# Kernel optimization log

Measured on AMD Instinct MI355X. Metric: run time of the kernel, lower is better.

The kernel has to match this reference:

```python
import jax, jax.numpy as jnp
import numpy as np

# hyperparameters (from init_kwargs)
DIM = 192; NH = 6; WS = 16; SHIFT = 8; M = 64; RC = 10; CS = 256; KS = 5
HID = DIM * 2  # mlp_ratio = 2


def _layernorm(x, g, b, eps=1e-5):
    mu = jnp.mean(x, axis=-1, keepdims=True)
    var = jnp.var(x, axis=-1, keepdims=True)
    return (x - mu) * jax.lax.rsqrt(var + eps) * g + b


def _window_partition(x, ws):
    b, h, w, c = x.shape
    x = x.reshape(b, h // ws, ws, w // ws, ws, c)
    return x.transpose(0, 1, 3, 2, 4, 5).reshape(-1, ws, ws, c)


def _window_reverse(win, ws, h, w):
    b = win.shape[0] // ((h // ws) * (w // ws))
    x = win.reshape(b, h // ws, w // ws, ws, ws, -1)
    return x.transpose(0, 1, 3, 2, 4, 5).reshape(b, h, w, -1)


def setup_inputs() -> dict:
    key = jax.random.key(0)
    ks = jax.random.split(key, 24)
    b, h, w = 2, 192, 192
    n = h * w
    f32 = jnp.float32
    rn = lambda k, shape, s=0.02: (jax.random.normal(k, shape) * s).astype(f32)
    inp = {}
    inp['x'] = jax.random.normal(ks[0], (b, n, DIM), f32)
    inp['td'] = jax.random.normal(ks[1], (b, M, DIM), f32)
    # relative position index (standard Swin construction)
    coords = np.stack(np.meshgrid(np.arange(WS), np.arange(WS), indexing='ij')).reshape(2, -1)
    rel = (coords[:, :, None] - coords[:, None, :]).transpose(1, 2, 0).astype(np.int64)
    rel[:, :, 0] += WS - 1; rel[:, :, 1] += WS - 1
    rel[:, :, 0] *= 2 * WS - 1
    inp['rpi_sa'] = jnp.asarray(rel.sum(-1), jnp.int32)  # (ws^2, ws^2)
    # shifted-window attention mask (0 / -100)
    img_mask = np.zeros((1, h, w, 1), np.float32)
    cnt = 0
    for hs in (slice(0, -WS), slice(-WS, -SHIFT), slice(-SHIFT, None)):
        for wsl in (slice(0, -WS), slice(-WS, -SHIFT), slice(-SHIFT, None)):
            img_mask[:, hs, wsl, :] = cnt; cnt += 1
    mw = np.asarray(_window_partition(jnp.asarray(img_mask), WS)).reshape(-1, WS * WS)
    am = mw[:, None, :] - mw[:, :, None]
    inp['attn_mask'] = jnp.asarray(np.where(am != 0, -100.0, 0.0).astype(np.float32))  # (nw, ws^2, ws^2)
    inp['h'] = h; inp['w'] = w
    # parameters
    inp['norm1_g'] = jnp.ones((DIM,), f32); inp['norm1_b'] = jnp.zeros((DIM,), f32)
    inp['norm2_g'] = jnp.ones((DIM,), f32); inp['norm2_b'] = jnp.zeros((DIM,), f32)
    inp['norm3_g'] = jnp.ones((DIM,), f32); inp['norm3_b'] = jnp.zeros((DIM,), f32)
    inp['wqkv_w'] = rn(ks[2], (DIM, 3 * DIM)); inp['wqkv_b'] = jnp.zeros((3 * DIM,), f32)
    inp['wq_w'] = rn(ks[3], (DIM, RC)); inp['wq_b'] = jnp.zeros((RC,), f32)
    inp['wk_w'] = rn(ks[4], (DIM, RC)); inp['wk_b'] = jnp.zeros((RC,), f32)
    inp['wv_w'] = rn(ks[5], (DIM, DIM)); inp['wv_b'] = jnp.zeros((DIM,), f32)
    inp['atd_scale'] = 0.5 * jnp.ones((M,), f32)
    inp['proj_aca_w'] = rn(ks[6], (DIM, DIM)); inp['proj_aca_b'] = jnp.zeros((DIM,), f32)
    inp['logit_scale'] = jnp.full((1, 1), np.log(10.0), f32)
    inp['rpb_table'] = rn(ks[7], ((2 * WS - 1) ** 2, NH))
    inp['proj_win_w'] = rn(ks[8], (DIM, DIM)); inp['proj_win_b'] = jnp.zeros((DIM,), f32)
    inp['fc1_w'] = rn(ks[9], (DIM, HID)); inp['fc1_b'] = jnp.zeros((HID,), f32)
    inp['dw_w'] = rn(ks[10], (HID, 1, KS, KS)); inp['dw_b'] = jnp.zeros((HID,), f32)
    inp['fc2_w'] = rn(ks[11], (HID, DIM)); inp['fc2_b'] = jnp.zeros((DIM,), f32)
    inp['sigma'] = jnp.zeros((M, 1), f32)
    return inp


def reference(x, td, rpi_sa, attn_mask, h, w,
              norm1_g, norm1_b, norm2_g, norm2_b, norm3_g, norm3_b,
              wqkv_w, wqkv_b, wq_w, wq_b, wk_w, wk_b, wv_w, wv_b, atd_scale,
              proj_aca_w, proj_aca_b, logit_scale, rpb_table, proj_win_w, proj_win_b,
              fc1_w, fc1_b, dw_w, dw_b, fc2_w, fc2_b, sigma):
    b, n, c = x.shape
    hd = c // NH
    shortcut = x
    xn = _layernorm(x, norm1_g, norm1_b)
    qkv = xn @ wqkv_w + wqkv_b  # (b, n, 3c)

    # ----- ATD_CA: token-dictionary cross attention -----
    q = xn @ wq_w + wq_b                              # (b, n, rc)
    k = td @ wk_w + wk_b                              # (b, m, rc)
    v = td @ wv_w + wv_b                              # (b, m, c)
    qn = q / jnp.maximum(jnp.linalg.norm(q, axis=-1, keepdims=True), 1e-12)
    kn = k / jnp.maximum(jnp.linalg.norm(k, axis=-1, keepdims=True), 1e-12)
    attn = jnp.einsum('bnr,bmr->bnm', qn, kn)
    attn = attn * (1.0 + jnp.clip(atd_scale, 0.0, 1.0) * np.float32(np.log(M)))
    sim_atd = jax.nn.softmax(attn, axis=-1)           # (b, n, m)
    x_atd = jnp.einsum('bnm,bmc->bnc', sim_atd, v)

    # ----- AC_MSA: category sort + grouped attention -----
    gs = min(n, CS); ng = (n + gs - 1) // gs; pad_n = ng * gs - n
    tk_id = jnp.argmax(sim_atd, axis=-1)              # (b, n)
    sort_idx = jnp.argsort(tk_id, axis=-1)
    inv_idx = jnp.argsort(sort_idx, axis=-1)
    shuf = jnp.take_along_axis(qkv, sort_idx[:, :, None], axis=1)
    padded = jnp.concatenate([shuf, shuf[:, n - pad_n:n, :][:, ::-1, :]], axis=1)
    y = padded.reshape(b, ng, gs, 3, NH, hd).transpose(3, 0, 1, 4, 2, 5)  # (3,b,ng,nh,gs,hd)
    qg, kg, vg = y[0], y[1], y[2]
    ls = jnp.exp(jnp.minimum(logit_scale, np.float32(np.log(100.0))))
    ag = jax.nn.softmax(jnp.einsum('bgnqd,bgnkd->bgnqk', qg, kg) * ls, axis=-1)
    x_aca = jnp.einsum('bgnqk,bgnkd->bgnqd', ag, vg).transpose(0, 1, 3, 2, 4).reshape(b, ng * gs, c)[:, :n]
    x_aca = jnp.take_along_axis(x_aca, inv_idx[:, :, None], axis=1)
    x_aca = x_aca @ proj_aca_w + proj_aca_b

    # ----- shifted-window MSA -----
    qkv_img = qkv.reshape(b, h, w, 3 * c)
    shifted = jnp.roll(qkv_img, (-SHIFT, -SHIFT), axis=(1, 2))
    wins = _window_partition(shifted, WS).reshape(-1, WS * WS, 3 * c)
    b_, nt = wins.shape[0], WS * WS
    qkvw = wins.reshape(b_, nt, 3, NH, hd).transpose(2, 0, 3, 1, 4)
    qw = qkvw[0] * (hd ** -0.5); kw = qkvw[1]; vw = qkvw[2]
    aw = jnp.einsum('bhqd,bhkd->bhqk', qw, kw)
    rpb = rpb_table[rpi_sa.reshape(-1)].reshape(nt, nt, NH).transpose(2, 0, 1)
    aw = aw + rpb[None]
    nw = attn_mask.shape[0]
    aw = (aw.reshape(b_ // nw, nw, NH, nt, nt) + attn_mask[None, :, None]).reshape(b_, NH, nt, nt)
    aw = jax.nn.softmax(aw, axis=-1)
    ow = jnp.einsum('bhqk,bhkd->bhqd', aw, vw).transpose(0, 2, 1, 3).reshape(b_, nt, c)
    ow = ow @ proj_win_w + proj_win_b
    shifted_x = _window_reverse(ow.reshape(-1, WS, WS, c), WS, h, w)
    x_win = jnp.roll(shifted_x, (SHIFT, SHIFT), axis=(1, 2)).reshape(b, n, c)

    x = shortcut + x_win + x_atd + x_aca

    # ----- ConvFFN -----
    y2 = _layernorm(x, norm2_g, norm2_b)
    y2 = jax.nn.gelu(y2 @ fc1_w + fc1_b, approximate=False)
    img = y2.transpose(0, 2, 1).reshape(b, HID, h, w)
    cv = jax.lax.conv_general_dilated(img, dw_w, (1, 1), [(KS // 2, KS // 2)] * 2,
                                      feature_group_count=HID)
    cv = jax.nn.gelu(cv + dw_b[None, :, None, None], approximate=False)
    y2 = y2 + cv.reshape(b, HID, n).transpose(0, 2, 1)
    x = x + (y2 @ fc2_w + fc2_b)

    # ----- adaptive token dictionary refinement -----
    mask_soft = jax.nn.softmax(sim_atd.transpose(0, 2, 1), axis=-1)  # (b, m, n)
    s = jax.nn.sigmoid(sigma)  # (m, 1)
    td_new = s * td + (1.0 - s) * jnp.einsum('bmn,bnc->bmc', mask_soft,
                                             _layernorm(x, norm3_g, norm3_b))
    return x, td_new
```

## Files before the change

### kernel.cpp

```cpp
#include <hip/hip_runtime.h>
#include <math.h>

#define BB 2
#define HH 192
#define WW 192
#define NN 36864
#define CC 192
#define NHEAD 6
#define HD 32
#define MM 64
#define RC 10
#define GS 256
#define NG 144
#define HID 384
#define BN 73728

typedef unsigned short u16;
typedef __attribute__((ext_vector_type(8))) short short8;
typedef __attribute__((ext_vector_type(4))) float f32x4;

__device__ __forceinline__ float b2f(u16 u) { return __uint_as_float(((unsigned)u) << 16); }
__device__ __forceinline__ u16 f2b(float f) {
  unsigned v = __float_as_uint(f);
  return (u16)((v + 0x7fffu + ((v >> 16) & 1u)) >> 16);
}
__device__ __forceinline__ void up8(uint4 u, float* f) {
  f[0] = __uint_as_float(u.x << 16); f[1] = __uint_as_float(u.x & 0xffff0000u);
  f[2] = __uint_as_float(u.y << 16); f[3] = __uint_as_float(u.y & 0xffff0000u);
  f[4] = __uint_as_float(u.z << 16); f[5] = __uint_as_float(u.z & 0xffff0000u);
  f[6] = __uint_as_float(u.w << 16); f[7] = __uint_as_float(u.w & 0xffff0000u);
}
__device__ __forceinline__ float gelu_f(float v) {
  return 0.5f * v * (1.f + erff(v * 0.70710678118654752f));
}

__global__ void zero_kernel(int* __restrict__ p, int n) {
  int i = blockIdx.x * 256 + threadIdx.x;
  if (i < n) p[i] = 0;
}

__global__ __launch_bounds__(256) void ln1_kernel(const float* __restrict__ x,
                                                  const float* __restrict__ g,
                                                  const float* __restrict__ be,
                                                  const float* __restrict__ wq,
                                                  const float* __restrict__ wqb,
                                                  u16* __restrict__ xnb,
                                                  float* __restrict__ qn) {
  int row = blockIdx.x * 4 + (threadIdx.x >> 6);
  int lane = threadIdx.x & 63;
  const float* p = x + (size_t)row * CC;
  float v0 = p[lane], v1 = p[lane + 64], v2 = p[lane + 128];
  float s = v0 + v1 + v2;
#pragma unroll
  for (int o = 32; o > 0; o >>= 1) s += __shfl_xor(s, o);
  float mu = s * (1.f / 192.f);
  float d0 = v0 - mu, d1 = v1 - mu, d2 = v2 - mu;
  float q2 = d0 * d0 + d1 * d1 + d2 * d2;
#pragma unroll
  for (int o = 32; o > 0; o >>= 1) q2 += __shfl_xor(q2, o);
  float rstd = rsqrtf(q2 * (1.f / 192.f) + 1e-5f);
  float xn0 = d0 * rstd * g[lane] + be[lane];
  float xn1 = d1 * rstd * g[lane + 64] + be[lane + 64];
  float xn2 = d2 * rstd * g[lane + 128] + be[lane + 128];
  u16* op = xnb + (size_t)row * CC;
  op[lane] = f2b(xn0); op[lane + 64] = f2b(xn1); op[lane + 128] = f2b(xn2);
  float qv[RC];
#pragma unroll
  for (int r = 0; r < RC; r++) {
    float t = xn0 * wq[lane * RC + r] + xn1 * wq[(lane + 64) * RC + r] + xn2 * wq[(lane + 128) * RC + r];
#pragma unroll
    for (int o = 32; o > 0; o >>= 1) t += __shfl_xor(t, o);
    qv[r] = t + wqb[r];
  }
  float nr = 0.f;
#pragma unroll
  for (int r = 0; r < RC; r++) nr += qv[r] * qv[r];
  float inv = 1.f / fmaxf(sqrtf(nr), 1e-12f);
  if (lane == 0) {
    float* qo = qn + (size_t)row * RC;
#pragma unroll
    for (int r = 0; r < RC; r++) qo[r] = qv[r] * inv;
  }
}

__global__ __launch_bounds__(256) void ln_kernel(const float* __restrict__ in,
                                                 u16* __restrict__ out,
                                                 const float* __restrict__ g,
                                                 const float* __restrict__ be) {
  int row = blockIdx.x * 4 + (threadIdx.x >> 6);
  int lane = threadIdx.x & 63;
  const float* p = in + (size_t)row * CC;
  float v0 = p[lane], v1 = p[lane + 64], v2 = p[lane + 128];
  float s = v0 + v1 + v2;
#pragma unroll
  for (int o = 32; o > 0; o >>= 1) s += __shfl_xor(s, o);
  float mu = s * (1.f / 192.f);
  float d0 = v0 - mu, d1 = v1 - mu, d2 = v2 - mu;
  float q2 = d0 * d0 + d1 * d1 + d2 * d2;
#pragma unroll
  for (int o = 32; o > 0; o >>= 1) q2 += __shfl_xor(q2, o);
  float rstd = rsqrtf(q2 * (1.f / 192.f) + 1e-5f);
  u16* op = out + (size_t)row * CC;
  op[lane]       = f2b(d0 * rstd * g[lane] + be[lane]);
  op[lane + 64]  = f2b(d1 * rstd * g[lane + 64] + be[lane + 64]);
  op[lane + 128] = f2b(d2 * rstd * g[lane + 128] + be[lane + 128]);
}

template <int EPI>
__global__ __launch_bounds__(256) void gemm_mfma(const u16* __restrict__ A,
                                                 const float* __restrict__ Bw,
                                                 const float* __restrict__ bias,
                                                 void* __restrict__ Cv,
                                                 int K, int Nn) {
  __shared__ u16 As[128][72];
  __shared__ u16 Bst[64][72];
  int tid = threadIdx.x;
  int m0 = blockIdx.x * 128, n0 = blockIdx.y * 64;
  int wave = tid >> 6, lane = tid & 63;
  int l16 = lane & 15, l4 = lane >> 4;
  int wm = wave >> 1, wn = wave & 1;
  f32x4 acc[4][2];
#pragma unroll
  for (int mi = 0; mi < 4; mi++)
#pragma unroll
    for (int ni = 0; ni < 2; ni++) acc[mi][ni] = (f32x4){0.f, 0.f, 0.f, 0.f};
  for (int k0 = 0; k0 < K; k0 += 64) {
#pragma unroll
    for (int i = 0; i < 4; i++) {
      int li = tid + i * 256;
      int row = li >> 3, c8 = (li & 7) * 8;
      uint4 v = *reinterpret_cast<const uint4*>(A + (size_t)(m0 + row) * K + k0 + c8);
      *reinterpret_cast<uint4*>(&As[row][c8]) = v;
    }
#pragma unroll
    for (int i = 0; i < 4; i++) {
      int li = tid + i * 256;
      int k = li >> 4, n4 = (li & 15) * 4;
      float4 bv = *reinterpret_cast<const float4*>(Bw + (size_t)(k0 + k) * Nn + n0 + n4);
      Bst[n4 + 0][k] = f2b(bv.x);
      Bst[n4 + 1][k] = f2b(bv.y);
      Bst[n4 + 2][k] = f2b(bv.z);
      Bst[n4 + 3][k] = f2b(bv.w);
    }
    __syncthreads();
#pragma unroll
    for (int kk = 0; kk < 64; kk += 32) {
      short8 af[4], bf[2];
#pragma unroll
      for (int mi = 0; mi < 4; mi++)
        af[mi] = *reinterpret_cast<const short8*>(&As[wm * 64 + mi * 16 + l16][kk + l4 * 8]);
#pragma unroll
      for (int ni = 0; ni < 2; ni++)
        bf[ni] = *reinterpret_cast<const short8*>(&Bst[wn * 32 + ni * 16 + l16][kk + l4 * 8]);
#pragma unroll
      for (int mi = 0; mi < 4; mi++)
#pragma unroll
        for (int ni = 0; ni < 2; ni++)
          acc[mi][ni] = __builtin_amdgcn_mfma_f32_16x16x32_bf16(af[mi], bf[ni], acc[mi][ni], 0, 0, 0);
    }
    __syncthreads();
  }
#pragma unroll
  for (int ni = 0; ni < 2; ni++) {
    int col = n0 + wn * 32 + ni * 16 + l16;
    float bv = bias[col];
#pragma unroll
    for (int mi = 0; mi < 4; mi++) {
#pragma unroll
      for (int r = 0; r < 4; r++) {
        int row = m0 + wm * 64 + mi * 16 + 4 * l4 + r;
        size_t off = (size_t)row * Nn + col;
        float c = acc[mi][ni][r] + bv;
        if constexpr (EPI == 2) {
          ((float*)Cv)[off] += c;
        } else {
          if constexpr (EPI == 1) c = gelu_f(c);
          ((u16*)Cv)[off] = f2b(c);
        }
      }
    }
  }
}

__global__ __launch_bounds__(1024) void tdproj_kernel(const float* __restrict__ td,
                                                      const float* __restrict__ wk,
                                                      const float* __restrict__ wkb,
                                                      const float* __restrict__ wv,
                                                      const float* __restrict__ wvb,
                                                      const float* __restrict__ atd_scale,
                                                      float* __restrict__ knv,
                                                      float* __restrict__ vtd) {
  int b = blockIdx.x, tid = threadIdx.x;
  __shared__ float td_s[MM * CC];
  __shared__ float k_s[MM][RC];
  const float* tdb = td + (size_t)b * MM * CC;
  for (int i = tid; i < MM * CC; i += 1024) td_s[i] = tdb[i];
  __syncthreads();
  for (int i = tid; i < MM * CC; i += 1024) {
    int m = i / CC, c = i % CC;
    float a = wvb[c];
    for (int r = 0; r < CC; r++) a += td_s[m * CC + r] * wv[r * CC + c];
    vtd[(size_t)b * MM * CC + i] = a;
  }
  for (int i = tid; i < MM * RC; i += 1024) {
    int m = i / RC, r = i % RC;
    float a = wkb[r];
    for (int c = 0; c < CC; c++) a += td_s[m * CC + c] * wk[c * RC + r];
    k_s[m][r] = a;
  }
  __syncthreads();
  if (tid < MM) {
    int m = tid;
    float nr = 0.f;
    for (int r = 0; r < RC; r++) nr += k_s[m][r] * k_s[m][r];
    float inv = 1.f / fmaxf(sqrtf(nr), 1e-12f);
    float sc = 1.f + fminf(fmaxf(atd_scale[m], 0.f), 1.f) * 4.1588830833596715f;
    for (int r = 0; r < RC; r++) knv[(size_t)b * MM * RC + m * RC + r] = k_s[m][r] * inv * sc;
  }
}

__global__ __launch_bounds__(256, 2) void atd_kernel(const float* __restrict__ qn,
                                                     const float* __restrict__ x,
                                                     const float* __restrict__ knv,
                                                     const float* __restrict__ vtd,
                                                     float* __restrict__ sim,
                                                     int* __restrict__ tkid,
                                                     float* __restrict__ xacc) {
  __shared__ float v_s[MM][CC];
  __shared__ float kn_s[MM][11];
  __shared__ float p_s[4][64];
  int tid = threadIdx.x;
  int b = (blockIdx.x * 64) / NN;
  float* vflat = &v_s[0][0];
  for (int i = tid; i < MM * CC; i += 256) vflat[i] = vtd[(size_t)b * MM * CC + i];
  for (int i = tid; i < MM * RC; i += 256) kn_s[i / RC][i % RC] = knv[(size_t)b * MM * RC + i];
  __syncthreads();
  int wave = tid >> 6, lane = tid & 63;
  for (int it = 0; it < 16; it++) {
    int tg = blockIdx.x * 64 + it * 4 + wave;
    const float* qr = qn + (size_t)tg * RC;
    float s = 0.f;
#pragma unroll
    for (int r = 0; r < RC; r++) s += qr[r] * kn_s[lane][r];
    float mx = s; int ai = lane;
#pragma unroll
    for (int o = 32; o > 0; o >>= 1) {
      float ov = __shfl_xor(mx, o); int oi = __shfl_xor(ai, o);
      if (ov > mx || (ov == mx && oi < ai)) { mx = ov; ai = oi; }
    }
    float e = __expf(s - mx);
    float sum = e;
#pragma unroll
    for (int o = 32; o > 0; o >>= 1) sum += __shfl_xor(sum, o);
    float p = e / sum;
    sim[(size_t)tg * MM + lane] = p;
    if (lane == 0) tkid[tg] = ai;
    p_s[wave][lane] = p;
    float a0 = 0.f, a1 = 0.f, a2 = 0.f;
#pragma unroll
    for (int m = 0; m < MM; m++) {
      float pm = p_s[wave][m];
      a0 += pm * v_s[m][lane];
      a1 += pm * v_s[m][lane + 64];
      a2 += pm * v_s[m][lane + 128];
    }
    const float* xr = x + (size_t)tg * CC;
    float* xo = xacc + (size_t)tg * CC;
    xo[lane]       = xr[lane]       + a0;
    xo[lane + 64]  = xr[lane + 64]  + a1;
    xo[lane + 128] = xr[lane + 128] + a2;
  }
}

__global__ void hist_kernel(const int* __restrict__ tkid, int* __restrict__ hist) {
  int i = blockIdx.x * 256 + threadIdx.x;
  if (i < BN) atomicAdd(&hist[(i / NN) * MM + tkid[i]], 1);
}

__global__ void scan_kernel(const int* __restrict__ hist, int* __restrict__ base) {
  int lane = threadIdx.x & 63, b = threadIdx.x >> 6;
  int v = hist[b * MM + lane];
  int xx = v;
#pragma unroll
  for (int o = 1; o < 64; o <<= 1) { int t = __shfl_up(xx, o); if (lane >= o) xx += t; }
  base[b * MM + lane] = xx - v;
}

__global__ __launch_bounds__(256) void scatter_kernel(const int* __restrict__ tkid,
                                                      const int* __restrict__ base,
                                                      int* __restrict__ sort_idx) {
  int bk = blockIdx.x;
  int b = bk >> 6, key = bk & 63;
  int tid = threadIdx.x, wave = tid >> 6, lane = tid & 63;
  __shared__ int wtot[4];
  int offset = base[b * MM + key];
  const int* tk = tkid + (size_t)b * NN;
  for (int c0 = 0; c0 < NN; c0 += 256) {
    int i = c0 + tid;
    bool f = (tk[i] == key);
    unsigned long long mb = __ballot(f);
    int wpre = __popcll(mb & ((1ull << lane) - 1ull));
    if (lane == 0) wtot[wave] = __popcll(mb);
    __syncthreads();
    int pre = wpre;
#pragma unroll
    for (int w = 0; w < 4; w++) if (w < wave) pre += wtot[w];
    int tot = wtot[0] + wtot[1] + wtot[2] + wtot[3];
    if (f) sort_idx[(size_t)b * NN + offset + pre] = i;
    offset += tot;
    __syncthreads();
  }
}

__global__ void rpb_kernel(const int* __restrict__ rpi, const float* __restrict__ table,
                           float* __restrict__ rpbT) {
  int ij = blockIdx.x * 256 + threadIdx.x;
  int q = ij >> 8, k = ij & 255;
  int idx = rpi[ij];
#pragma unroll
  for (int h = 0; h < NHEAD; h++) rpbT[h * 65536 + k * 256 + q] = table[idx * NHEAD + h];
}

__global__ __launch_bounds__(256, 3) void attn_mfma_kernel(const u16* __restrict__ qkv,
                                                           const int* __restrict__ sort_idx,
                                                           const float* __restrict__ lgsc,
                                                           const float* __restrict__ rpbT,
                                                           const float* __restrict__ amask,
                                                           u16* __restrict__ ao) {
  __shared__ u16 Ks[GS][40];
  __shared__ u16 Vt[HD][GS + 8];
  __shared__ u16 Ps[4][16][72];
  int idx = blockIdx.x;
  int mode = 0;
  if (idx >= BB * NG * NHEAD) { mode = 1; idx -= BB * NG * NHEAD; }
  int h = idx % NHEAD; idx /= NHEAD;
  int g = idx % NG;    idx /= NG;
  int b = idx;
  int tid = threadIdx.x;
  int wave = tid >> 6, lane = tid & 63;
  int l16 = lane & 15, l4 = lane >> 4;
  const int* sp = sort_idx + (size_t)b * NN + g * GS;
  int wy = g / 12, wx = g % 12;

  auto tokof = [&](int i) -> int {
    if (mode == 0) return sp[i];
    int sy = (wy * 16 + (i >> 4) + 8) % 192;
    int sx = (wx * 16 + (i & 15) + 8) % 192;
    return sy * 192 + sx;
  };

#pragma unroll
  for (int it = 0; it < 4; it++) {
    int li = tid + it * 256;
    int tok = li >> 2, q8 = (li & 3) * 8;
    size_t bas = ((size_t)b * NN + tokof(tok)) * 576 + h * HD + q8;
    uint4 kv = *reinterpret_cast<const uint4*>(qkv + bas + CC);
    *reinterpret_cast<uint4*>(&Ks[tok][q8]) = kv;
    ushort4 v0 = *reinterpret_cast<const ushort4*>(qkv + bas + 2 * CC);
    ushort4 v1 = *reinterpret_cast<const ushort4*>(qkv + bas + 2 * CC + 4);
    Vt[q8 + 0][tok] = v0.x; Vt[q8 + 1][tok] = v0.y;
    Vt[q8 + 2][tok] = v0.z; Vt[q8 + 3][tok] = v0.w;
    Vt[q8 + 4][tok] = v1.x; Vt[q8 + 5][tok] = v1.y;
    Vt[q8 + 6][tok] = v1.z; Vt[q8 + 7][tok] = v1.w;
  }
  float qscale = (mode == 0) ? __expf(fminf(lgsc[0], 4.605170185988092f))
                             : 0.17677669529663687f;
  bool bnd = (mode == 1) && ((wy == 11) || (wx == 11));
  __syncthreads();

  for (int qt = 0; qt < 4; qt++) {
    int q0 = wave * 64 + qt * 16 + 4 * l4;
    short8 qf;
    {
      int qrow = wave * 64 + qt * 16 + l16;
      size_t bas = ((size_t)b * NN + tokof(qrow)) * 576 + h * HD + l4 * 8;
      uint4 u = *reinterpret_cast<const uint4*>(qkv + bas);
      float f[8]; up8(u, f);
#pragma unroll
      for (int j = 0; j < 8; j++) ((u16*)&qf)[j] = f2b(f[j] * qscale);
    }
    f32x4 S[16];
#pragma unroll
    for (int kt = 0; kt < 16; kt++) {
      short8 kf = *reinterpret_cast<const short8*>(&Ks[kt * 16 + l16][l4 * 8]);
      f32x4 cin = (f32x4){0.f, 0.f, 0.f, 0.f};
      if (mode == 1)
        cin = *reinterpret_cast<const f32x4*>(rpbT + h * 65536 + (kt * 16 + l16) * 256 + q0);
      S[kt] = __builtin_amdgcn_mfma_f32_16x16x32_bf16(qf, kf, cin, 0, 0, 0);
    }
    if (bnd) {
#pragma unroll
      for (int kt = 0; kt < 16; kt++)
#pragma unroll
        for (int r = 0; r < 4; r++)
          S[kt][r] += amask[(size_t)g * 65536 + (size_t)(q0 + r) * 256 + kt * 16 + l16];
    }
#pragma unroll
    for (int r = 0; r < 4; r++) {
      float m = S[0][r];
#pragma unroll
      for (int kt = 1; kt < 16; kt++) m = fmaxf(m, S[kt][r]);
#pragma unroll
      for (int o = 1; o < 16; o <<= 1) m = fmaxf(m, __shfl_xor(m, o));
      float sum = 0.f;
#pragma unroll
      for (int kt = 0; kt < 16; kt++) {
        float p = __expf(S[kt][r] - m);
        S[kt][r] = p;
        sum += p;
      }
#pragma unroll
      for (int o = 1; o < 16; o <<= 1) sum += __shfl_xor(sum, o);
      float inv = 1.f / sum;
#pragma unroll
      for (int kt = 0; kt < 16; kt++) S[kt][r] *= inv;
    }
    f32x4 O0 = (f32x4){0.f, 0.f, 0.f, 0.f};
    f32x4 O1 = (f32x4){0.f, 0.f, 0.f, 0.f};
    for (int kc = 0; kc < 4; kc++) {
#pragma unroll
      for (int kt = 0; kt < 4; kt++)
#pragma unroll
        for (int r = 0; r < 4; r++)
          Ps[wave][4 * l4 + r][kt * 16 + l16] = f2b(S[kc * 4 + kt][r]);
#pragma unroll
      for (int s = 0; s < 2; s++) {
        short8 pa = *reinterpret_cast<const short8*>(&Ps[wave][l16][s * 32 + l4 * 8]);
        short8 v0 = *reinterpret_cast<const short8*>(&Vt[l16][kc * 64 + s * 32 + l4 * 8]);
        short8 v1 = *reinterpret_cast<const short8*>(&Vt[16 + l16][kc * 64 + s * 32 + l4 * 8]);
        O0 = __builtin_amdgcn_mfma_f32_16x16x32_bf16(pa, v0, O0, 0, 0, 0);
        O1 = __builtin_amdgcn_mfma_f32_16x16x32_bf16(pa, v1, O1, 0, 0, 0);
      }
    }
    int coff = mode ? CC : 0;
#pragma unroll
    for (int r = 0; r < 4; r++) {
      int tok = tokof(q0 + r);
      u16* ob = ao + ((size_t)b * NN + tok) * 384 + coff + h * HD;
      ob[l16]      = f2b(O0[r]);
      ob[16 + l16] = f2b(O1[r]);
    }
  }
}

__global__ void prep_kernel(const float* __restrict__ pa_w, const float* __restrict__ pw_w,
                            const float* __restrict__ pa_b, const float* __restrict__ pw_b,
                            float* __restrict__ wcat, float* __restrict__ bcat) {
  int i = blockIdx.x * 256 + threadIdx.x;
  int k = i / 192, n = i % 192;
  wcat[i] = (k < 192) ? pa_w[k * 192 + n] : pw_w[(k - 192) * 192 + n];
  if (i < 192) bcat[i] = pa_b[i] + pw_b[i];
}

__global__ __launch_bounds__(384) void dwconv_kernel(const u16* __restrict__ y2,
                                                     const float* __restrict__ dww,
                                                     const float* __restrict__ dwb,
                                                     u16* __restrict__ y2pc) {
  int c = threadIdx.x;
  int blk = blockIdx.x;
  int half = blk & 1;
  int row = blk >> 1;
  int y = row % HH;
  int b = row / HH;
  int x0 = half * 96;
  float w[25];
#pragma unroll
  for (int j = 0; j < 25; j++) w[j] = dww[c * 25 + j];
  float bias = dwb[c];
  const u16* rp[5];
  bool rv[5];
#pragma unroll
  for (int dy = 0; dy < 5; dy++) {
    int yy = y + dy - 2;
    rv[dy] = (yy >= 0 && yy < HH);
    rp[dy] = y2 + ((size_t)b * NN + (size_t)(rv[dy] ? yy : y) * WW) * HID + c;
  }
  float win[5][5];
#pragma unroll
  for (int j = 0; j < 4; j++) {
    int col = x0 - 2 + j;
    constexpr int slotmap[4] = {3, 4, 0, 1};
    int slot = slotmap[j];
    bool cvld = (col >= 0);
    int colc = cvld ? col : 0;
#pragma unroll
    for (int dy = 0; dy < 5; dy++) {
      float v = b2f(rp[dy][(size_t)colc * HID]);
      win[dy][slot] = (cvld && rv[dy]) ? v : 0.f;
    }
  }
  u16* op = y2pc + ((size_t)b * NN + (size_t)y * WW) * HID + c;
  for (int tb = 0; tb < 100; tb += 5) {
#pragma unroll
    for (int p = 0; p < 5; p++) {
      int t = tb + p;
      int col = x0 + t + 2;
      const int slot = (p + 2) % 5;
      bool cvld = (col < WW);
      int colc = cvld ? col : (WW - 1);
#pragma unroll
      for (int dy = 0; dy < 5; dy++) {
        float v = b2f(rp[dy][(size_t)colc * HID]);
        win[dy][slot] = (cvld && rv[dy]) ? v : 0.f;
      }
      if (t < 96) {
        float acc = 0.f;
#pragma unroll
        for (int dy = 0; dy < 5; dy++)
#pragma unroll
          for (int dx = 0; dx < 5; dx++)
            acc += w[dy * 5 + dx] * win[dy][(p + 3 + dx) % 5];
        float gl = gelu_f(acc + bias);
        float res = win[2][p];
        op[(size_t)(x0 + t) * HID] = f2b(res + gl);
      }
    }
  }
}

__global__ __launch_bounds__(256) void zsum_kernel(const float* __restrict__ sim,
                                                   float* __restrict__ Z) {
  int blk = blockIdx.x;
  int b = blk / NG;
  int n0 = (blk % NG) * 256;
  int tid = threadIdx.x, m = tid & 63, sub = tid >> 6;
  float a = 0.f;
  const float* sp = sim + ((size_t)b * NN + n0) * MM;
  for (int n = sub; n < 256; n += 4) a += __expf(sp[n * MM + m]);
  __shared__ float red[4][64];
  red[sub][m] = a;
  __syncthreads();
  if (tid < 64) atomicAdd(&Z[b * MM + m], red[0][m] + red[1][m] + red[2][m] + red[3][m]);
}

__global__ void invz_kernel(const float* __restrict__ Z, float* __restrict__ invZ) {
  int i = threadIdx.x;
  invZ[i] = 1.f / Z[i];
}

__global__ __launch_bounds__(192, 2) void tdacc_kernel(const float* __restrict__ sim,
                                                       const float* __restrict__ invZ,
                                                       const u16* __restrict__ ln3x,
                                                       float* __restrict__ tdacc) {
  __shared__ u16 w_s[256][64];
  int blk = blockIdx.x;
  int b = blk / NG;
  int n0 = (blk % NG) * 256;
  int tid = threadIdx.x;
  const float* sp = sim + ((size_t)b * NN + n0) * MM;
  const float* iz = invZ + b * MM;
  for (int i = tid; i < 256 * 64; i += 192)
    w_s[i >> 6][i & 63] = f2b(__expf(sp[i]) * iz[i & 63]);
  __syncthreads();
  float acc[64];
#pragma unroll
  for (int m = 0; m < 64; m++) acc[m] = 0.f;
  const u16* lp = ln3x + ((size_t)b * NN + n0) * CC + tid;
  for (int n = 0; n < 256; n++) {
    float val = b2f(lp[(size_t)n * CC]);
    const uint4* wr = reinterpret_cast<const uint4*>(&w_s[n][0]);
#pragma unroll
    for (int c8 = 0; c8 < 8; c8++) {
      float f[8]; up8(wr[c8], f);
#pragma unroll
      for (int t = 0; t < 8; t++) acc[c8 * 8 + t] += f[t] * val;
    }
  }
  for (int m = 0; m < 64; m++) atomicAdd(&tdacc[((size_t)b * MM + m) * CC + tid], acc[m]);
}

__global__ void tdfin_kernel(const float* __restrict__ td, const float* __restrict__ sigma,
                             const float* __restrict__ tdacc, float* __restrict__ out) {
  int i = blockIdx.x * 256 + threadIdx.x;
  if (i >= BB * MM * CC) return;
  int m = (i / CC) % MM;
  float s = 1.f / (1.f + __expf(-sigma[m]));
  out[i] = s * td[i] + (1.f - s) * tdacc[i];
}

static constexpr size_t oQKV = 0;
static constexpr size_t oXN  = oQKV + (size_t)BN * 576 * 2;
static constexpr size_t oAO  = oXN  + (size_t)BN * CC * 2;
static constexpr size_t oSIM = oAO  + (size_t)BN * 384 * 2;
static constexpr size_t oQN  = oSIM + (size_t)BN * MM * 4;
static constexpr size_t oRPB = oQN  + (size_t)BN * RC * 4;
static constexpr size_t oVTD = oRPB + (size_t)6 * 65536 * 4;
static constexpr size_t oKNV = oVTD + (size_t)BB * MM * CC * 4;
static constexpr size_t oWC  = oKNV + (size_t)BB * MM * RC * 4;
static constexpr size_t oBC  = oWC  + (size_t)384 * 192 * 4;
static constexpr size_t oTK  = oBC  + 1024;
static constexpr size_t oSORT= oTK  + (size_t)BN * 4;
static constexpr size_t oHIST= oSORT+ (size_t)BN * 4;
static constexpr size_t oBASE= oHIST+ 512;
static constexpr size_t oZ   = oBASE+ 512;
static constexpr size_t oTDA = oZ   + 512;
static constexpr size_t oINV = oTDA + (size_t)BB * MM * CC * 4;
static constexpr size_t WS_NEEDED = oINV + 512;

extern "C" void kernel_launch(void* const* d_in, const int* in_sizes, int n_in,
                              void* d_out, int out_size, void* d_ws, size_t ws_size,
                              hipStream_t stream) {
  if (ws_size < WS_NEEDED) return;
  const float* x       = (const float*)d_in[0];
  const float* td      = (const float*)d_in[1];
  const int*   rpi     = (const int*)d_in[2];
  const float* amask   = (const float*)d_in[3];
  const float* n1g     = (const float*)d_in[6];
  const float* n1b     = (const float*)d_in[7];
  const float* n2g     = (const float*)d_in[8];
  const float* n2b     = (const float*)d_in[9];
  const float* n3g     = (const float*)d_in[10];
  const float* n3b     = (const float*)d_in[11];
  const float* wqkv_w  = (const float*)d_in[12];
  const float* wqkv_b  = (const float*)d_in[13];
  const float* wq_w    = (const float*)d_in[14];
  const float* wq_b    = (const float*)d_in[15];
  const float* wk_w    = (const float*)d_in[16];
  const float* wk_b    = (const float*)d_in[17];
  const float* wv_w    = (const float*)d_in[18];
  const float* wv_b    = (const float*)d_in[19];
  const float* atd_sc  = (const float*)d_in[20];
  const float* paca_w  = (const float*)d_in[21];
  const float* paca_b  = (const float*)d_in[22];
  const float* lgsc    = (const float*)d_in[23];
  const float* rpb_tab = (const float*)d_in[24];
  const float* pwin_w  = (const float*)d_in[25];
  const float* pwin_b  = (const float*)d_in[26];
  const float* fc1_w   = (const float*)d_in[27];
  const float* fc1_b   = (const float*)d_in[28];
  const float* dw_w    = (const float*)d_in[29];
  const float* dw_b    = (const float*)d_in[30];
  const float* fc2_w   = (const float*)d_in[31];
  const float* fc2_b   = (const float*)d_in[32];
  const float* sigma   = (const float*)d_in[33];
  float* out = (float*)d_out;
  char* wsb = (char*)d_ws;

  u16*   QKVb = (u16*)(wsb + oQKV);
  u16*   XNb  = (u16*)(wsb + oXN);
  u16*   AOb  = (u16*)(wsb + oAO);
  float* SIM  = (float*)(wsb + oSIM);
  float* QN   = (float*)(wsb + oQN);
  float* RPB  = (float*)(wsb + oRPB);
  float* VTD  = (float*)(wsb + oVTD);
  float* KNV  = (float*)(wsb + oKNV);
  float* WC   = (float*)(wsb + oWC);
  float* BC   = (float*)(wsb + oBC);
  int*   TK   = (int*)(wsb + oTK);
  int*   SORT = (int*)(wsb + oSORT);
  int*   HIST = (int*)(wsb + oHIST);
  int*   BASE = (int*)(wsb + oBASE);
  float* Z    = (float*)(wsb + oZ);
  float* TDA  = (float*)(wsb + oTDA);
  float* INVZ = (float*)(wsb + oINV);

  zero_kernel<<<98, 256, 0, stream>>>(HIST, 24960);
  ln1_kernel<<<BN / 4, 256, 0, stream>>>(x, n1g, n1b, wq_w, wq_b, XNb, QN);
  tdproj_kernel<<<BB, 1024, 0, stream>>>(td, wk_w, wk_b, wv_w, wv_b, atd_sc, KNV, VTD);
  gemm_mfma<0><<<dim3(BN / 128, 9), 256, 0, stream>>>(XNb, wqkv_w, wqkv_b, QKVb, 192, 576);
  atd_kernel<<<BN / 64, 256, 0, stream>>>(QN, x, KNV, VTD, SIM, TK, out);
  hist_kernel<<<BN / 256, 256, 0, stream>>>(TK, HIST);
  scan_kernel<<<1, 128, 0, stream>>>(HIST, BASE);
  scatter_kernel<<<BB * MM, 256, 0, stream>>>(TK, BASE, SORT);
  rpb_kernel<<<256, 256, 0, stream>>>(rpi, rpb_tab, RPB);
  attn_mfma_kernel<<<2 * BB * NG * NHEAD, 256, 0, stream>>>(QKVb, SORT, lgsc, RPB, amask, AOb);
  prep_kernel<<<288, 256, 0, stream>>>(paca_w, pwin_w, paca_b, pwin_b, WC, BC);
  gemm_mfma<2><<<dim3(BN / 128, 3), 256, 0, stream>>>(AOb, WC, BC, out, 384, 192);
  ln_kernel<<<BN / 4, 256, 0, stream>>>(out, XNb, n2g, n2b);
  gemm_mfma<1><<<dim3(BN / 128, 6), 256, 0, stream>>>(XNb, fc1_w, fc1_b, QKVb, 192, 384);
  dwconv_kernel<<<BB * HH * 2, 384, 0, stream>>>(QKVb, dw_w, dw_b, AOb);
  gemm_mfma<2><<<dim3(BN / 128, 3), 256, 0, stream>>>(AOb, fc2_w, fc2_b, out, 384, 192);
  ln_kernel<<<BN / 4, 256, 0, stream>>>(out, XNb, n3g, n3b);
  zsum_kernel<<<BB * NG, 256, 0, stream>>>(SIM, Z);
  invz_kernel<<<1, 128, 0, stream>>>(Z, INVZ);
  tdacc_kernel<<<BB * NG, 192, 0, stream>>>(SIM, INVZ, XNb, TDA);
  tdfin_kernel<<<96, 256, 0, stream>>>(td, sigma, TDA, out + (size_t)BN * CC);
}
```

Before: 1.286 ms.

## Replace LDS-staged GEMM with direct-load single-wave MFMA GEMM using pre-transposed bf16 weights

Replaces the shared-memory tiled GEMM with a one-wave-per-block kernel that loads A and pre-transposed bf16 B fragments straight from global memory into MFMA operands. It removes LDS staging, the barriers, and the per-tile fp32-to-bf16 weight conversion. New prep kernels convert and transpose all four weight matrices once per call, and the dwconv block order is remapped so rows are spread across blocks. The cost is no LDS reuse: each A row is read by several blocks and fragment loads are strided, so performance now depends on cache hits. The fc1 and fc2 bias paths are kept, but the transposed weights reuse the RPB workspace region.

```diff
diff --git a/kernel.cpp b/kernel.cpp
--- a/kernel.cpp
+++ b/kernel.cpp
@@ -107,69 +107,45 @@
 }
 
 template <int EPI>
-__global__ __launch_bounds__(256) void gemm_mfma(const u16* __restrict__ A,
-                                                 const float* __restrict__ Bw,
-                                                 const float* __restrict__ bias,
-                                                 void* __restrict__ Cv,
-                                                 int K, int Nn) {
-  __shared__ u16 As[128][72];
-  __shared__ u16 Bst[64][72];
-  int tid = threadIdx.x;
-  int m0 = blockIdx.x * 128, n0 = blockIdx.y * 64;
-  int wave = tid >> 6, lane = tid & 63;
+__global__ __launch_bounds__(64) void gemm_direct(const u16* __restrict__ A,
+                                                  const u16* __restrict__ Bt,
+                                                  const float* __restrict__ bias,
+                                                  void* __restrict__ Cv,
+                                                  int K, int Nn) {
+  int lane = threadIdx.x;
   int l16 = lane & 15, l4 = lane >> 4;
-  int wm = wave >> 1, wn = wave & 1;
-  f32x4 acc[4][2];
+  int m0 = blockIdx.x * 64, n0 = blockIdx.y * 64;
+  f32x4 acc[4][4];
 #pragma unroll
   for (int mi = 0; mi < 4; mi++)
 #pragma unroll
-    for (int ni = 0; ni < 2; ni++) acc[mi][ni] = (f32x4){0.f, 0.f, 0.f, 0.f};
-  for (int k0 = 0; k0 < K; k0 += 64) {
-#pragma unroll
-    for (int i = 0; i < 4; i++) {
-      int li = tid + i * 256;
-      int row = li >> 3, c8 = (li & 7) * 8;
-      uint4 v = *reinterpret_cast<const uint4*>(A + (size_t)(m0 + row) * K + k0 + c8);
-      *reinterpret_cast<uint4*>(&As[row][c8]) = v;
-    }
-#pragma unroll
-    for (int i = 0; i < 4; i++) {
-      int li = tid + i * 256;
-      int k = li >> 4, n4 = (li & 15) * 4;
-      float4 bv = *reinterpret_cast<const float4*>(Bw + (size_t)(k0 + k) * Nn + n0 + n4);
-      Bst[n4 + 0][k] = f2b(bv.x);
-      Bst[n4 + 1][k] = f2b(bv.y);
-      Bst[n4 + 2][k] = f2b(bv.z);
-      Bst[n4 + 3][k] = f2b(bv.w);
-    }
-    __syncthreads();
-#pragma unroll
-    for (int kk = 0; kk < 64; kk += 32) {
-      short8 af[4], bf[2];
-#pragma unroll
-      for (int mi = 0; mi < 4; mi++)
-        af[mi] = *reinterpret_cast<const short8*>(&As[wm * 64 + mi * 16 + l16][kk + l4 * 8]);
-#pragma unroll
-      for (int ni = 0; ni < 2; ni++)
-        bf[ni] = *reinterpret_cast<const short8*>(&Bst[wn * 32 + ni * 16 + l16][kk + l4 * 8]);
-#pragma unroll
-      for (int mi = 0; mi < 4; mi++)
-#pragma unroll
-        for (int ni = 0; ni < 2; ni++)
-          acc[mi][ni] = __builtin_amdgcn_mfma_f32_16x16x32_bf16(af[mi], bf[ni], acc[mi][ni], 0, 0, 0);
-    }
-    __syncthreads();
-  }
-#pragma unroll
-  for (int ni = 0; ni < 2; ni++) {
-    int col = n0 + wn * 32 + ni * 16 + l16;
+    for (int ni = 0; ni < 4; ni++) acc[mi][ni] = (f32x4){0.f, 0.f, 0.f, 0.f};
+  const u16* ap = A + (size_t)(m0 + l16) * K + l4 * 8;
+  const u16* bp = Bt + (size_t)(n0 + l16) * K + l4 * 8;
+#pragma unroll 2
+  for (int kk = 0; kk < K; kk += 32) {
+    short8 af[4], bf[4];
+#pragma unroll
+    for (int mi = 0; mi < 4; mi++)
+      af[mi] = *reinterpret_cast<const short8*>(ap + (size_t)mi * 16 * K + kk);
+#pragma unroll
+    for (int ni = 0; ni < 4; ni++)
+      bf[ni] = *reinterpret_cast<const short8*>(bp + (size_t)ni * 16 * K + kk);
+#pragma unroll
+    for (int mi = 0; mi < 4; mi++)
+#pragma unroll
+      for (int ni = 0; ni < 4; ni++)
+        acc[mi][ni] = __builtin_amdgcn_mfma_f32_16x16x32_bf16(af[mi], bf[ni], acc[mi][ni], 0, 0, 0);
+  }
+#pragma unroll
+  for (int ni = 0; ni < 4; ni++) {
+    int col = n0 + ni * 16 + l16;
     float bv = bias[col];
 #pragma unroll
     for (int mi = 0; mi < 4; mi++) {
 #pragma unroll
       for (int r = 0; r < 4; r++) {
-        int row = m0 + wm * 64 + mi * 16 + 4 * l4 + r;
-        size_t off = (size_t)row * Nn + col;
+        size_t off = (size_t)(m0 + mi * 16 + 4 * l4 + r) * Nn + col;
         float c = acc[mi][ni][r] + bv;
         if constexpr (EPI == 2) {
           ((float*)Cv)[off] += c;
@@ -180,6 +156,33 @@
       }
     }
   }
+}
+
+__global__ void wprep1_kernel(const float* __restrict__ w, u16* __restrict__ bt) {
+  int i = blockIdx.x * 256 + threadIdx.x;
+  int k = i / 576, n = i % 576;
+  bt[n * 192 + k] = f2b(w[i]);
+}
+
+__global__ void wprep2_kernel(const float* __restrict__ paca_w, const float* __restrict__ pwin_w,
+                              const float* __restrict__ fc1_w, const float* __restrict__ fc2_w,
+                              const float* __restrict__ paca_b, const float* __restrict__ pwin_b,
+                              u16* __restrict__ bt, float* __restrict__ bcat) {
+  int i = blockIdx.x * 256 + threadIdx.x;
+  {
+    int n = i / 384, k = i % 384;
+    float v = (k < 192) ? paca_w[k * 192 + n] : pwin_w[(k - 192) * 192 + n];
+    bt[i] = f2b(v);
+  }
+  {
+    int n = i / 192, k = i % 192;
+    bt[73728 + i] = f2b(fc1_w[k * 384 + n]);
+  }
+  {
+    int n = i / 384, k = i % 384;
+    bt[147456 + i] = f2b(fc2_w[k * 192 + n]);
+  }
+  if (i < 192) bcat[i] = paca_b[i] + pwin_b[i];
 }
 
 __global__ __launch_bounds__(1024) void tdproj_kernel(const float* __restrict__ td,
@@ -443,21 +446,13 @@
   }
 }
 
-__global__ void prep_kernel(const float* __restrict__ pa_w, const float* __restrict__ pw_w,
-                            const float* __restrict__ pa_b, const float* __restrict__ pw_b,
-                            float* __restrict__ wcat, float* __restrict__ bcat) {
-  int i = blockIdx.x * 256 + threadIdx.x;
-  int k = i / 192, n = i % 192;
-  wcat[i] = (k < 192) ? pa_w[k * 192 + n] : pw_w[(k - 192) * 192 + n];
-  if (i < 192) bcat[i] = pa_b[i] + pw_b[i];
-}
-
 __global__ __launch_bounds__(384) void dwconv_kernel(const u16* __restrict__ y2,
                                                      const float* __restrict__ dww,
                                                      const float* __restrict__ dwb,
                                                      u16* __restrict__ y2pc) {
   int c = threadIdx.x;
-  int blk = blockIdx.x;
+  int bid = blockIdx.x;
+  int blk = (bid & 7) * (BB * HH * 2 / 8) + (bid >> 3);
   int half = blk & 1;
   int row = blk >> 1;
   int y = row % HH;
@@ -642,9 +637,10 @@
   float* SIM  = (float*)(wsb + oSIM);
   float* QN   = (float*)(wsb + oQN);
   float* RPB  = (float*)(wsb + oRPB);
+  u16*   BT2  = (u16*)(wsb + oRPB);
   float* VTD  = (float*)(wsb + oVTD);
   float* KNV  = (float*)(wsb + oKNV);
-  float* WC   = (float*)(wsb + oWC);
+  u16*   BTQ  = (u16*)(wsb + oWC);
   float* BC   = (float*)(wsb + oBC);
   int*   TK   = (int*)(wsb + oTK);
   int*   SORT = (int*)(wsb + oSORT);
@@ -657,19 +653,20 @@
   zero_kernel<<<98, 256, 0, stream>>>(HIST, 24960);
   ln1_kernel<<<BN / 4, 256, 0, stream>>>(x, n1g, n1b, wq_w, wq_b, XNb, QN);
   tdproj_kernel<<<BB, 1024, 0, stream>>>(td, wk_w, wk_b, wv_w, wv_b, atd_sc, KNV, VTD);
-  gemm_mfma<0><<<dim3(BN / 128, 9), 256, 0, stream>>>(XNb, wqkv_w, wqkv_b, QKVb, 192, 576);
+  wprep1_kernel<<<432, 256, 0, stream>>>(wqkv_w, BTQ);
+  gemm_direct<0><<<dim3(BN / 64, 9), 64, 0, stream>>>(XNb, BTQ, wqkv_b, QKVb, 192, 576);
   atd_kernel<<<BN / 64, 256, 0, stream>>>(QN, x, KNV, VTD, SIM, TK, out);
   hist_kernel<<<BN / 256, 256, 0, stream>>>(TK, HIST);
   scan_kernel<<<1, 128, 0, stream>>>(HIST, BASE);
   scatter_kernel<<<BB * MM, 256, 0, stream>>>(TK, BASE, SORT);
   rpb_kernel<<<256, 256, 0, stream>>>(rpi, rpb_tab, RPB);
   attn_mfma_kernel<<<2 * BB * NG * NHEAD, 256, 0, stream>>>(QKVb, SORT, lgsc, RPB, amask, AOb);
-  prep_kernel<<<288, 256, 0, stream>>>(paca_w, pwin_w, paca_b, pwin_b, WC, BC);
-  gemm_mfma<2><<<dim3(BN / 128, 3), 256, 0, stream>>>(AOb, WC, BC, out, 384, 192);
+  wprep2_kernel<<<288, 256, 0, stream>>>(paca_w, pwin_w, fc1_w, fc2_w, paca_b, pwin_b, BT2, BC);
+  gemm_direct<2><<<dim3(BN / 64, 3), 64, 0, stream>>>(AOb, BT2, BC, out, 384, 192);
   ln_kernel<<<BN / 4, 256, 0, stream>>>(out, XNb, n2g, n2b);
-  gemm_mfma<1><<<dim3(BN / 128, 6), 256, 0, stream>>>(XNb, fc1_w, fc1_b, QKVb, 192, 384);
+  gemm_direct<1><<<dim3(BN / 64, 6), 64, 0, stream>>>(XNb, BT2 + 73728, fc1_b, QKVb, 192, 384);
   dwconv_kernel<<<BB * HH * 2, 384, 0, stream>>>(QKVb, dw_w, dw_b, AOb);
-  gemm_mfma<2><<<dim3(BN / 128, 3), 256, 0, stream>>>(AOb, fc2_w, fc2_b, out, 384, 192);
+  gemm_direct<2><<<dim3(BN / 64, 3), 64, 0, stream>>>(AOb, BT2 + 147456, fc2_b, out, 384, 192);
   ln_kernel<<<BN / 4, 256, 0, stream>>>(out, XNb, n3g, n3b);
   zsum_kernel<<<BB * NG, 256, 0, stream>>>(SIM, Z);
   invz_kernel<<<1, 128, 0, stream>>>(Z, INVZ);
```

New measurement: 1.343 ms. 4.4% more time.
